# Kernel optimization log

Hardware: AMD Instinct MI355X
Metric: run time of the kernel (lower is better)

Reference implementation:

```python
import jax, jax.numpy as jnp
import numpy as np

N_NODES = 50000
N_EDGES = 800000
D = 128
L = 3


def setup_inputs() -> dict:
    key = jax.random.key(0)
    ks = jax.random.split(key, 16)
    x = jax.random.normal(ks[0], (N_NODES, D), dtype=jnp.float32)
    edge_index = jax.random.randint(ks[1], (2, N_EDGES), 0, N_NODES, dtype=jnp.int32)
    # ensure every node has at least one incoming edge (degree > 0)
    edge_index = edge_index.at[1, :N_NODES].set(jnp.arange(N_NODES, dtype=jnp.int32))
    edge_attr = jax.random.normal(ks[2], (N_EDGES, 1), dtype=jnp.float32)
    s = 1.0 / np.sqrt(D)
    lin_w = jax.random.normal(ks[3], (L, 1, D), dtype=jnp.float32)          # edge_dim=1 -> D
    lin_b = jax.random.normal(ks[4], (L, D), dtype=jnp.float32) * s
    eps = jnp.zeros((L,), dtype=jnp.float32)                                 # initial_eps = 0, trainable
    w1 = jax.random.normal(ks[5], (L, D, D), dtype=jnp.float32) * s
    b1 = jax.random.normal(ks[6], (L, D), dtype=jnp.float32) * s
    w2 = jax.random.normal(ks[7], (L, D, D), dtype=jnp.float32) * s
    b2 = jax.random.normal(ks[8], (L, D), dtype=jnp.float32) * s
    d_cat = D + L * D
    final_w = jax.random.normal(ks[9], (d_cat, D), dtype=jnp.float32) / np.sqrt(d_cat)
    final_b = jax.random.normal(ks[10], (D,), dtype=jnp.float32) * s
    return {"x": x, "edge_index": edge_index, "edge_attr": edge_attr,
            "lin_w": lin_w, "lin_b": lin_b, "eps": eps,
            "w1": w1, "b1": b1, "w2": w2, "b2": b2,
            "final_w": final_w, "final_b": final_b}


def reference(x, edge_index, edge_attr, lin_w, lin_b, eps, w1, b1, w2, b2, final_w, final_b):
    src, tgt = edge_index[0], edge_index[1]
    n = x.shape[0]
    # degree of target nodes (float), shape [N, 1]
    deg = jax.ops.segment_sum(jnp.ones(src.shape[0], x.dtype), tgt, num_segments=n)[:, None]
    xs = [x]
    h = x
    for l in range(L):
        e = edge_attr @ lin_w[l] + lin_b[l]                  # [E, D] edge-feature projection
        msg = jax.nn.relu(h[src] + e)                        # gather + fuse + relu
        agg = jax.ops.segment_sum(msg, tgt, num_segments=n)  # scatter-add
        out = agg / deg + (1.0 + eps[l]) * h                 # degree-normalize + eps-residual
        h = jax.nn.relu(out @ w1[l] + b1[l]) @ w2[l] + b2[l] # 2-layer MLP (no BN, no dropout)
        xs.append(h)
    cat = jnp.concatenate(xs, axis=-1)                       # [N, D + L*D]
    return cat @ final_w + final_b
```

## Files before the change

kernel.cpp:

```cpp
#include <hip/hip_runtime.h>

#define NN 50000
#define NE 800000
#define DIM 128
#define NLAYERS 3

typedef __attribute__((ext_vector_type(8))) short bf16x8;
typedef __attribute__((ext_vector_type(4))) float f32x4;

__device__ __forceinline__ unsigned short f2bf_hi(float f) {
    unsigned int u = __float_as_uint(f);
    u += 0x7FFF + ((u >> 16) & 1);
    return (unsigned short)(u >> 16);
}
__device__ __forceinline__ float bf2f(unsigned short u) {
    return __uint_as_float(((unsigned int)u) << 16);
}

__global__ __launch_bounds__(256) void rank_kernel(const int* __restrict__ tgt,
                                                   int* __restrict__ counts,
                                                   int* __restrict__ rank, int E) {
    int base = (blockIdx.x * 256 + threadIdx.x) * 4;
    if (base >= E) return;
    int4 t = *(const int4*)(tgt + base);
    int4 r;
    r.x = atomicAdd(&counts[t.x], 1);
    r.y = atomicAdd(&counts[t.y], 1);
    r.z = atomicAdd(&counts[t.z], 1);
    r.w = atomicAdd(&counts[t.w], 1);
    *(int4*)(rank + base) = r;
}

__global__ __launch_bounds__(256) void scan_partial_kernel(const int* __restrict__ counts,
                                                           int* __restrict__ psum, int n) {
    __shared__ int ws[4];
    int b = blockIdx.x, t = threadIdx.x;
    int idx = b * 1024 + t * 4;
    int v = 0;
    if (idx < n) {
        int4 c = *(const int4*)(counts + idx);
        v = c.x + c.y + c.z + c.w;
    }
#pragma unroll
    for (int o = 32; o > 0; o >>= 1) v += __shfl_xor(v, o);
    int lane = t & 63, wid = t >> 6;
    if (lane == 0) ws[wid] = v;
    __syncthreads();
    if (t == 0) psum[b] = ws[0] + ws[1] + ws[2] + ws[3];
}

__global__ __launch_bounds__(64) void scan_small_kernel(const int* __restrict__ psum,
                                                        int* __restrict__ pbase,
                                                        int* __restrict__ offsets,
                                                        int nb, int n) {
    int lane = threadIdx.x;
    int v = (lane < nb) ? psum[lane] : 0;
    int incl = v;
#pragma unroll
    for (int o = 1; o < 64; o <<= 1) {
        int t = __shfl_up(incl, o);
        if (lane >= o) incl += t;
    }
    if (lane < nb) pbase[lane] = incl - v;
    if (lane == 63) offsets[n] = incl;
}

__global__ __launch_bounds__(256) void scan_apply_kernel(const int* __restrict__ counts,
                                                         const int* __restrict__ pbase,
                                                         int* __restrict__ offsets, int n) {
    __shared__ int ws[4];
    int b = blockIdx.x, t = threadIdx.x;
    int lane = t & 63, wid = t >> 6;
    int idx = b * 1024 + t * 4;
    int4 c = make_int4(0, 0, 0, 0);
    if (idx < n) c = *(const int4*)(counts + idx);
    int tsum = c.x + c.y + c.z + c.w;
    int incl = tsum;
#pragma unroll
    for (int o = 1; o < 64; o <<= 1) {
        int tt = __shfl_up(incl, o);
        if (lane >= o) incl += tt;
    }
    if (lane == 63) ws[wid] = incl;
    __syncthreads();
    int wbase = pbase[b];
    for (int w = 0; w < wid; w++) wbase += ws[w];
    if (idx < n) {
        int e0 = wbase + incl - tsum;
        int4 o;
        o.x = e0;
        o.y = e0 + c.x;
        o.z = o.y + c.y;
        o.w = o.z + c.z;
        *(int4*)(offsets + idx) = o;
    }
}

__global__ __launch_bounds__(256) void scatter2_kernel(
    const int* __restrict__ src, const int* __restrict__ tgt,
    const float* __restrict__ ea, const int* __restrict__ rank,
    const int* __restrict__ offsets, int2* __restrict__ sedge, int E) {
    int base = (blockIdx.x * 256 + threadIdx.x) * 4;
    if (base >= E) return;
    int4 s = *(const int4*)(src + base);
    int4 t = *(const int4*)(tgt + base);
    int4 r = *(const int4*)(rank + base);
    float4 a = *(const float4*)(ea + base);
    sedge[offsets[t.x] + r.x] = make_int2(s.x << 8, __float_as_int(a.x));
    sedge[offsets[t.y] + r.y] = make_int2(s.y << 8, __float_as_int(a.y));
    sedge[offsets[t.z] + r.z] = make_int2(s.z << 8, __float_as_int(a.z));
    sedge[offsets[t.w] + r.w] = make_int2(s.w << 8, __float_as_int(a.w));
}

__global__ __launch_bounds__(256) void xcvt_kernel(const float* __restrict__ x,
                                                   unsigned short* __restrict__ xb, int n) {
    int i = (blockIdx.x * 256 + threadIdx.x) * 4;
    if (i >= n) return;
    float4 v = *(const float4*)(x + i);
    ushort4 o;
    o.x = f2bf_hi(v.x); o.y = f2bf_hi(v.y);
    o.z = f2bf_hi(v.z); o.w = f2bf_hi(v.w);
    *(ushort4*)(xb + i) = o;
}

__global__ __launch_bounds__(256, 8) void agg_kernel(
    const unsigned short* __restrict__ hprev, const int* __restrict__ offs,
    const int2* __restrict__ sedge,
    const float* __restrict__ lw, const float* __restrict__ lb,
    const float* __restrict__ epsp, int layer,
    unsigned short* __restrict__ aggh, unsigned short* __restrict__ aggl, int N) {
    int g = threadIdx.x >> 4;
    int r = threadIdx.x & 15;
    int node = blockIdx.x * 16 + g;
    if (node >= N) return;
    int d0 = r * 8;
    float lwv[8], lbv[8];
    *(float4*)&lwv[0] = *(const float4*)(lw + d0);
    *(float4*)&lwv[4] = *(const float4*)(lw + d0 + 4);
    *(float4*)&lbv[0] = *(const float4*)(lb + d0);
    *(float4*)&lbv[4] = *(const float4*)(lb + d0 + 4);
    const char* hb = (const char*)hprev + r * 16;

    int s0 = offs[node], s1 = offs[node + 1];
    int sm = s1 - 1;
    int cnt = s1 - s0;
    float a[8];
#pragma unroll
    for (int c = 0; c < 8; c++) a[c] = 0.f;

    int2 e0 = sedge[s0];
    int2 e1 = sedge[min(s0 + 1, sm)];
    int2 e2 = sedge[min(s0 + 2, sm)];
    int2 e3 = sedge[min(s0 + 3, sm)];
    uint4 h0 = *(const uint4*)(hb + (unsigned)e0.x);
    uint4 h1 = *(const uint4*)(hb + (unsigned)e1.x);
    uint4 h2 = *(const uint4*)(hb + (unsigned)e2.x);

    for (int it = s0; it < s1; ++it) {
        uint4 h3 = *(const uint4*)(hb + (unsigned)e3.x);
        int2 e4 = sedge[min(it + 4, sm)];
        float wgt = __int_as_float(e0.y);
        unsigned uu[4] = {h0.x, h0.y, h0.z, h0.w};
#pragma unroll
        for (int c = 0; c < 4; c++) {
            float f0 = __uint_as_float(uu[c] << 16);
            float f1 = __uint_as_float(uu[c] & 0xffff0000u);
            a[2 * c]     += fmaxf(f0 + fmaf(wgt, lwv[2 * c], lbv[2 * c]), 0.f);
            a[2 * c + 1] += fmaxf(f1 + fmaf(wgt, lwv[2 * c + 1], lbv[2 * c + 1]), 0.f);
        }
        e0 = e1; e1 = e2; e2 = e3; e3 = e4;
        h0 = h1; h1 = h2; h2 = h3;
    }

    float inv = 1.f / (float)cnt;
    float ge = 1.f + epsp[layer];
    uint4 hs = *(const uint4*)(hb + ((unsigned)node << 8));
    unsigned su[4] = {hs.x, hs.y, hs.z, hs.w};
    unsigned short hh[8], hl[8];
#pragma unroll
    for (int c = 0; c < 4; c++) {
        float f0 = __uint_as_float(su[c] << 16);
        float f1 = __uint_as_float(su[c] & 0xffff0000u);
        float v0 = a[2 * c] * inv + ge * f0;
        float v1 = a[2 * c + 1] * inv + ge * f1;
        unsigned short h0v = f2bf_hi(v0), h1v = f2bf_hi(v1);
        hh[2 * c] = h0v; hh[2 * c + 1] = h1v;
        hl[2 * c] = f2bf_hi(v0 - bf2f(h0v));
        hl[2 * c + 1] = f2bf_hi(v1 - bf2f(h1v));
    }
    unsigned short* ph = aggh + (size_t)node * DIM + d0;
    unsigned short* pl = aggl + (size_t)node * DIM + d0;
    *(ushort4*)ph       = *(const ushort4*)&hh[0];
    *(ushort4*)(ph + 4) = *(const ushort4*)&hh[4];
    *(ushort4*)pl       = *(const ushort4*)&hl[0];
    *(ushort4*)(pl + 4) = *(const ushort4*)&hl[4];
}

__device__ __forceinline__ int packidx(int k, int c) {
    return (((k >> 5) << 3) + (c >> 4)) * 512 + (((k >> 3) & 3) << 7) + ((c & 15) << 3) + (k & 7);
}

__global__ __launch_bounds__(256) void wprep_kernel(
    const float* __restrict__ w1, const float* __restrict__ w2, const float* __restrict__ fw,
    unsigned short* __restrict__ w1t_h, unsigned short* __restrict__ w1t_l,
    unsigned short* __restrict__ w2t_h, unsigned short* __restrict__ w2t_l,
    unsigned short* __restrict__ fwt_h, unsigned short* __restrict__ fwt_l) {
    int gid = blockIdx.x * 256 + threadIdx.x;
    float v; int oidx;
    unsigned short *oh, *ol;
    if (gid < 49152) {
        int l = gid >> 14, rem = gid & 16383, k = rem >> 7, c = rem & 127;
        v = w1[gid]; oidx = l * 16384 + packidx(k, c); oh = w1t_h; ol = w1t_l;
    } else if (gid < 98304) {
        int g = gid - 49152;
        int l = g >> 14, rem = g & 16383, k = rem >> 7, c = rem & 127;
        v = w2[g]; oidx = l * 16384 + packidx(k, c); oh = w2t_h; ol = w2t_l;
    } else if (gid < 163840) {
        int g = gid - 98304;
        int k = g >> 7, c = g & 127;
        v = fw[g]; oidx = packidx(k, c); oh = fwt_h; ol = fwt_l;
    } else return;
    unsigned short h = f2bf_hi(v);
    float lo = v - bf2f(h);
    oh[oidx] = h;
    ol[oidx] = f2bf_hi(lo);
}

#define HSTR 136

#define MLP1_LOAD(T, Bh_, Bl_, Ah_, Al_) do {                               \
    int k0_ = (T) * 32;                                                     \
    _Pragma("unroll")                                                       \
    for (int j_ = 0; j_ < 2; j_++) {                                        \
        size_t ro_ = (size_t)rowc[j_] * DIM + k0_ + q * 8;                  \
        Bh_[j_] = *(const bf16x8*)(ah_g + ro_);                             \
        Bl_[j_] = *(const bf16x8*)(al_g + ro_);                             \
    }                                                                       \
    _Pragma("unroll")                                                       \
    for (int i_ = 0; i_ < 4; i_++) {                                        \
        size_t co_ = ((size_t)((T) * 8 + wr * 4 + i_) << 9) + lane * 8;     \
        Ah_[i_] = *(const bf16x8*)(w1h + co_);                              \
        Al_[i_] = *(const bf16x8*)(w1l + co_);                              \
    }                                                                       \
} while (0)

#define MLP2_LOADW(T, Ah_, Al_) do {                                        \
    _Pragma("unroll")                                                       \
    for (int i_ = 0; i_ < 4; i_++) {                                        \
        size_t co_ = ((size_t)((T) * 8 + wr * 4 + i_) << 9) + lane * 8;     \
        Ah_[i_] = *(const bf16x8*)(w2h + co_);                              \
        Al_[i_] = *(const bf16x8*)(w2l + co_);                              \
    }                                                                       \
} while (0)

#define MLP2_LOADB(T, Bh_, Bl_) do {                                        \
    int k0_ = (T) * 32;                                                     \
    _Pragma("unroll")                                                       \
    for (int j_ = 0; j_ < 2; j_++) {                                        \
        int so_ = (wc * 32 + j_ * 16 + lr) * HSTR + k0_ + q * 8;            \
        Bh_[j_] = *(const bf16x8*)&s_hh[so_];                               \
        Bl_[j_] = *(const bf16x8*)&s_hl[so_];                               \
    }                                                                       \
} while (0)

#define MLP_MFMA(Bh_, Bl_, Ah_, Al_) do {                                   \
    _Pragma("unroll")                                                       \
    for (int i_ = 0; i_ < 4; i_++)                                          \
        _Pragma("unroll")                                                   \
        for (int j_ = 0; j_ < 2; j_++) {                                    \
            acc[i_][j_] = __builtin_amdgcn_mfma_f32_16x16x32_bf16(Ah_[i_], Bh_[j_], acc[i_][j_], 0, 0, 0); \
            acc[i_][j_] = __builtin_amdgcn_mfma_f32_16x16x32_bf16(Ah_[i_], Bl_[j_], acc[i_][j_], 0, 0, 0); \
            acc[i_][j_] = __builtin_amdgcn_mfma_f32_16x16x32_bf16(Al_[i_], Bh_[j_], acc[i_][j_], 0, 0, 0); \
        }                                                                   \
} while (0)

__global__ __launch_bounds__(256, 3) void mlp_fused(
    const unsigned short* __restrict__ ah_g, const unsigned short* __restrict__ al_g,
    const unsigned short* __restrict__ w1h, const unsigned short* __restrict__ w1l,
    const float* __restrict__ b1,
    const unsigned short* __restrict__ w2h, const unsigned short* __restrict__ w2l,
    const float* __restrict__ b2,
    unsigned short* __restrict__ out, int N) {
    __shared__ unsigned short s_hh[64 * HSTR], s_hl[64 * HSTR];
    int tid = threadIdx.x;
    int lane = tid & 63, w = tid >> 6;
    int q = lane >> 4, lr = lane & 15;
    int wr = w >> 1, wc = w & 1;
    int n0 = blockIdx.x * 64;
    int nb0 = n0 + wc * 32 + lr;
    int rowc[2];
    rowc[0] = min(nb0, N - 1);
    rowc[1] = min(nb0 + 16, N - 1);

    f32x4 acc[4][2];
#pragma unroll
    for (int i = 0; i < 4; i++)
#pragma unroll
        for (int j = 0; j < 2; j++) acc[i][j] = (f32x4)(0.f);

    bf16x8 pBh[2], pBl[2], pAh[4], pAl[4];
    bf16x8 qBh[2], qBl[2], qAh[4], qAl[4];

    MLP1_LOAD(0, pBh, pBl, pAh, pAl);
    MLP1_LOAD(1, qBh, qBl, qAh, qAl);
    MLP_MFMA(pBh, pBl, pAh, pAl);
    MLP1_LOAD(2, pBh, pBl, pAh, pAl);
    MLP_MFMA(qBh, qBl, qAh, qAl);
    MLP1_LOAD(3, qBh, qBl, qAh, qAl);
    MLP_MFMA(pBh, pBl, pAh, pAl);
    MLP_MFMA(qBh, qBl, qAh, qAl);

    MLP2_LOADW(0, pAh, pAl);

#pragma unroll
    for (int i = 0; i < 4; i++) {
        int hc0 = wr * 64 + i * 16 + q * 4;
        float4 bv = *(const float4*)(b1 + hc0);
        float bvr[4] = {bv.x, bv.y, bv.z, bv.w};
#pragma unroll
        for (int j = 0; j < 2; j++) {
            int nl = wc * 32 + j * 16 + lr;
            unsigned short hh[4], hl[4];
#pragma unroll
            for (int r = 0; r < 4; r++) {
                float v = fmaxf(acc[i][j][r] + bvr[r], 0.f);
                unsigned short h = f2bf_hi(v);
                hh[r] = h;
                hl[r] = f2bf_hi(v - bf2f(h));
            }
            *(ushort4*)&s_hh[nl * HSTR + hc0] = *(const ushort4*)&hh[0];
            *(ushort4*)&s_hl[nl * HSTR + hc0] = *(const ushort4*)&hl[0];
        }
    }
    __syncthreads();

#pragma unroll
    for (int i = 0; i < 4; i++)
#pragma unroll
        for (int j = 0; j < 2; j++) acc[i][j] = (f32x4)(0.f);

    MLP2_LOADB(0, pBh, pBl);
    MLP2_LOADW(1, qAh, qAl);
    MLP2_LOADB(1, qBh, qBl);
    MLP_MFMA(pBh, pBl, pAh, pAl);
    MLP2_LOADW(2, pAh, pAl);
    MLP2_LOADB(2, pBh, pBl);
    MLP_MFMA(qBh, qBl, qAh, qAl);
    MLP2_LOADW(3, qAh, qAl);
    MLP2_LOADB(3, qBh, qBl);
    MLP_MFMA(pBh, pBl, pAh, pAl);
    MLP_MFMA(qBh, qBl, qAh, qAl);

#pragma unroll
    for (int i = 0; i < 4; i++) {
        int hc0 = wr * 64 + i * 16 + q * 4;
        float4 bv = *(const float4*)(b2 + hc0);
        float bvr[4] = {bv.x, bv.y, bv.z, bv.w};
#pragma unroll
        for (int j = 0; j < 2; j++) {
            int node = nb0 + j * 16;
            if (node < N) {
                unsigned short o[4];
#pragma unroll
                for (int r = 0; r < 4; r++) o[r] = f2bf_hi(acc[i][j][r] + bvr[r]);
                *(ushort4*)&out[(size_t)node * DIM + hc0] = *(const ushort4*)&o[0];
            }
        }
    }
}

#define FIN_LOAD(T, Bv_, Ah_, Al_) do {                                     \
    const unsigned short* asrc_ = srcs[(T) >> 2];                           \
    int kk_ = ((T) & 3) * 32;                                               \
    _Pragma("unroll")                                                       \
    for (int j_ = 0; j_ < 2; j_++) {                                        \
        size_t ro_ = (size_t)rowc[j_] * DIM + kk_ + q * 8;                  \
        Bv_[j_] = *(const bf16x8*)(asrc_ + ro_);                            \
    }                                                                       \
    _Pragma("unroll")                                                       \
    for (int i_ = 0; i_ < 4; i_++) {                                        \
        size_t co_ = ((size_t)((T) * 8 + wr * 4 + i_) << 9) + lane * 8;     \
        Ah_[i_] = *(const bf16x8*)(wh + co_);                               \
        Al_[i_] = *(const bf16x8*)(wl + co_);                               \
    }                                                                       \
} while (0)

#define FIN_MFMA(Bv_, Ah_, Al_) do {                                        \
    _Pragma("unroll")                                                       \
    for (int i_ = 0; i_ < 4; i_++)                                          \
        _Pragma("unroll")                                                   \
        for (int j_ = 0; j_ < 2; j_++) {                                    \
            acc[i_][j_] = __builtin_amdgcn_mfma_f32_16x16x32_bf16(Ah_[i_], Bv_[j_], acc[i_][j_], 0, 0, 0); \
            acc[i_][j_] = __builtin_amdgcn_mfma_f32_16x16x32_bf16(Al_[i_], Bv_[j_], acc[i_][j_], 0, 0, 0); \
        }                                                                   \
} while (0)

__global__ __launch_bounds__(256, 3) void final_mfma(
    const unsigned short* __restrict__ a0, const unsigned short* __restrict__ a1,
    const unsigned short* __restrict__ a2, const unsigned short* __restrict__ a3,
    const unsigned short* __restrict__ wh, const unsigned short* __restrict__ wl,
    const float* __restrict__ bias, float* __restrict__ out, int N) {
    int tid = threadIdx.x;
    int lane = tid & 63, w = tid >> 6;
    int q = lane >> 4, lr = lane & 15;
    int wr = w >> 1, wc = w & 1;
    int n0 = blockIdx.x * 64;
    int nb0 = n0 + wc * 32 + lr;
    const unsigned short* srcs[4] = {a0, a1, a2, a3};
    int rowc[2];
    rowc[0] = min(nb0, N - 1);
    rowc[1] = min(nb0 + 16, N - 1);

    f32x4 acc[4][2];
#pragma unroll
    for (int i = 0; i < 4; i++)
#pragma unroll
        for (int j = 0; j < 2; j++) acc[i][j] = (f32x4)(0.f);

    bf16x8 pB[2], pAh[4], pAl[4];
    bf16x8 qB[2], qAh[4], qAl[4];

    FIN_LOAD(0, pB, pAh, pAl);
    FIN_LOAD(1, qB, qAh, qAl);
#pragma unroll
    for (int t = 0; t < 16; t += 2) {
        FIN_MFMA(pB, pAh, pAl);
        if (t + 2 < 16) FIN_LOAD(t + 2, pB, pAh, pAl);
        FIN_MFMA(qB, qAh, qAl);
        if (t + 3 < 16) FIN_LOAD(t + 3, qB, qAh, qAl);
    }

#pragma unroll
    for (int i = 0; i < 4; i++) {
        int hc0 = wr * 64 + i * 16 + q * 4;
        float4 bv = *(const float4*)(bias + hc0);
        float bvr[4] = {bv.x, bv.y, bv.z, bv.w};
#pragma unroll
        for (int j = 0; j < 2; j++) {
            int node = nb0 + j * 16;
            if (node < N) {
                float4 o;
                o.x = acc[i][j][0] + bvr[0];
                o.y = acc[i][j][1] + bvr[1];
                o.z = acc[i][j][2] + bvr[2];
                o.w = acc[i][j][3] + bvr[3];
                *(float4*)&out[(size_t)node * DIM + hc0] = o;
            }
        }
    }
}

extern "C" void kernel_launch(void* const* d_in, const int* in_sizes, int n_in,
                              void* d_out, int out_size, void* d_ws, size_t ws_size,
                              hipStream_t stream) {
    const float* x   = (const float*)d_in[0];
    const int* edge_index = (const int*)d_in[1];
    const float* ea  = (const float*)d_in[2];
    const float* lw  = (const float*)d_in[3];
    const float* lb  = (const float*)d_in[4];
    const float* eps = (const float*)d_in[5];
    const float* w1  = (const float*)d_in[6];
    const float* b1  = (const float*)d_in[7];
    const float* w2  = (const float*)d_in[8];
    const float* b2  = (const float*)d_in[9];
    const float* fw  = (const float*)d_in[10];
    const float* fb  = (const float*)d_in[11];
    float* out = (float*)d_out;

    const int N = NN, E = NE;
    const int* src = edge_index;
    const int* tgt = edge_index + E;
    const int NB = (N + 1023) / 1024;

    char* ws = (char*)d_ws;
    size_t off = 0;
    auto alloc = [&](size_t bytes) {
        void* p = ws + off;
        off += (bytes + 255) & ~(size_t)255;
        return p;
    };
    int*   counts  = (int*)alloc((size_t)N * 4);
    int*   offsets = (int*)alloc((size_t)(N + 1) * 4);
    int*   rank    = (int*)alloc((size_t)E * 4);
    int*   psum    = (int*)alloc((size_t)NB * 4);
    int*   pbase   = (int*)alloc((size_t)NB * 4);
    int2*  sedge   = (int2*)alloc((size_t)E * 8);
    unsigned short* w1t_h = (unsigned short*)alloc(49152 * 2);
    unsigned short* w1t_l = (unsigned short*)alloc(49152 * 2);
    unsigned short* w2t_h = (unsigned short*)alloc(49152 * 2);
    unsigned short* w2t_l = (unsigned short*)alloc(49152 * 2);
    unsigned short* fwt_h = (unsigned short*)alloc(65536 * 2);
    unsigned short* fwt_l = (unsigned short*)alloc(65536 * 2);
    unsigned short* xb    = (unsigned short*)alloc((size_t)N * DIM * 2);
    unsigned short* hbuf[3];
    for (int i = 0; i < 3; i++) hbuf[i] = (unsigned short*)alloc((size_t)N * DIM * 2);
    unsigned short* aggh = (unsigned short*)alloc((size_t)N * DIM * 2);
    unsigned short* aggl = (unsigned short*)alloc((size_t)N * DIM * 2);
    (void)ws_size; (void)in_sizes; (void)n_in; (void)out_size;

    hipMemsetAsync(counts, 0, (size_t)N * 4, stream);
    rank_kernel<<<(E / 4 + 255) / 256, 256, 0, stream>>>(tgt, counts, rank, E);
    wprep_kernel<<<640, 256, 0, stream>>>(w1, w2, fw, w1t_h, w1t_l, w2t_h, w2t_l, fwt_h, fwt_l);
    xcvt_kernel<<<(N * DIM / 4 + 255) / 256, 256, 0, stream>>>(x, xb, N * DIM);
    scan_partial_kernel<<<NB, 256, 0, stream>>>(counts, psum, N);
    scan_small_kernel<<<1, 64, 0, stream>>>(psum, pbase, offsets, NB, N);
    scan_apply_kernel<<<NB, 256, 0, stream>>>(counts, pbase, offsets, N);
    scatter2_kernel<<<(E / 4 + 255) / 256, 256, 0, stream>>>(src, tgt, ea, rank, offsets, sedge, E);

    const int GB = (N + 63) / 64;
    const int AB = (N + 15) / 16;
    for (int l = 0; l < NLAYERS; l++) {
        const unsigned short* hin = (l == 0) ? xb : hbuf[l - 1];
        agg_kernel<<<AB, 256, 0, stream>>>(hin, offsets, sedge,
            lw + l * DIM, lb + l * DIM, eps, l, aggh, aggl, N);
        mlp_fused<<<GB, 256, 0, stream>>>(
            aggh, aggl,
            w1t_h + l * 16384, w1t_l + l * 16384, b1 + l * DIM,
            w2t_h + l * 16384, w2t_l + l * 16384, b2 + l * DIM,
            hbuf[l], N);
    }
    final_mfma<<<GB, 256, 0, stream>>>(
        xb, hbuf[0], hbuf[1], hbuf[2], fwt_h, fwt_l, fb, out, N);
}
```

Baseline: 366.3 us.

## Fuse last-layer MLP with final projection and merge prep kernels

The third layer's MLP now feeds the final concat-projection directly inside one kernel. The last hidden state stays in shared memory as hi/lo bf16 and is used with split precision for the last K-slices, so it is never written to or re-read from global memory. The x conversion and weight packing kernels are also merged into one launch. This removes a kernel launch and an N×128 round trip, at the cost of a longer kernel with more register and LDS pressure, and it gives the last hidden state higher precision than the earlier layers.

```diff
diff --git a/kernel.cpp b/kernel.cpp
--- a/kernel.cpp
+++ b/kernel.cpp
@@ -112,15 +112,47 @@
     sedge[offsets[t.w] + r.w] = make_int2(s.w << 8, __float_as_int(a.w));
 }
 
-__global__ __launch_bounds__(256) void xcvt_kernel(const float* __restrict__ x,
-                                                   unsigned short* __restrict__ xb, int n) {
-    int i = (blockIdx.x * 256 + threadIdx.x) * 4;
-    if (i >= n) return;
-    float4 v = *(const float4*)(x + i);
-    ushort4 o;
-    o.x = f2bf_hi(v.x); o.y = f2bf_hi(v.y);
-    o.z = f2bf_hi(v.z); o.w = f2bf_hi(v.w);
-    *(ushort4*)(xb + i) = o;
+__device__ __forceinline__ int packidx(int k, int c) {
+    return (((k >> 5) << 3) + (c >> 4)) * 512 + (((k >> 3) & 3) << 7) + ((c & 15) << 3) + (k & 7);
+}
+
+#define XCVT_T 1600000
+
+__global__ __launch_bounds__(256) void prep_kernel(
+    const float* __restrict__ x, unsigned short* __restrict__ xb,
+    const float* __restrict__ w1, const float* __restrict__ w2, const float* __restrict__ fw,
+    unsigned short* __restrict__ w1t_h, unsigned short* __restrict__ w1t_l,
+    unsigned short* __restrict__ w2t_h, unsigned short* __restrict__ w2t_l,
+    unsigned short* __restrict__ fwt_h, unsigned short* __restrict__ fwt_l) {
+    int gid = blockIdx.x * 256 + threadIdx.x;
+    if (gid < XCVT_T) {
+        int i = gid * 4;
+        float4 v = *(const float4*)(x + i);
+        ushort4 o;
+        o.x = f2bf_hi(v.x); o.y = f2bf_hi(v.y);
+        o.z = f2bf_hi(v.z); o.w = f2bf_hi(v.w);
+        *(ushort4*)(xb + i) = o;
+        return;
+    }
+    int g0 = gid - XCVT_T;
+    float v; int oidx;
+    unsigned short *oh, *ol;
+    if (g0 < 49152) {
+        int l = g0 >> 14, rem = g0 & 16383, k = rem >> 7, c = rem & 127;
+        v = w1[g0]; oidx = l * 16384 + packidx(k, c); oh = w1t_h; ol = w1t_l;
+    } else if (g0 < 98304) {
+        int g = g0 - 49152;
+        int l = g >> 14, rem = g & 16383, k = rem >> 7, c = rem & 127;
+        v = w2[g]; oidx = l * 16384 + packidx(k, c); oh = w2t_h; ol = w2t_l;
+    } else if (g0 < 163840) {
+        int g = g0 - 98304;
+        int k = g >> 7, c = g & 127;
+        v = fw[g]; oidx = packidx(k, c); oh = fwt_h; ol = fwt_l;
+    } else return;
+    unsigned short h = f2bf_hi(v);
+    float lo = v - bf2f(h);
+    oh[oidx] = h;
+    ol[oidx] = f2bf_hi(lo);
 }
 
 __global__ __launch_bounds__(256, 8) void agg_kernel(
@@ -196,36 +228,6 @@
     *(ushort4*)(pl + 4) = *(const ushort4*)&hl[4];
 }
 
-__device__ __forceinline__ int packidx(int k, int c) {
-    return (((k >> 5) << 3) + (c >> 4)) * 512 + (((k >> 3) & 3) << 7) + ((c & 15) << 3) + (k & 7);
-}
-
-__global__ __launch_bounds__(256) void wprep_kernel(
-    const float* __restrict__ w1, const float* __restrict__ w2, const float* __restrict__ fw,
-    unsigned short* __restrict__ w1t_h, unsigned short* __restrict__ w1t_l,
-    unsigned short* __restrict__ w2t_h, unsigned short* __restrict__ w2t_l,
-    unsigned short* __restrict__ fwt_h, unsigned short* __restrict__ fwt_l) {
-    int gid = blockIdx.x * 256 + threadIdx.x;
-    float v; int oidx;
-    unsigned short *oh, *ol;
-    if (gid < 49152) {
-        int l = gid >> 14, rem = gid & 16383, k = rem >> 7, c = rem & 127;
-        v = w1[gid]; oidx = l * 16384 + packidx(k, c); oh = w1t_h; ol = w1t_l;
-    } else if (gid < 98304) {
-        int g = gid - 49152;
-        int l = g >> 14, rem = g & 16383, k = rem >> 7, c = rem & 127;
-        v = w2[g]; oidx = l * 16384 + packidx(k, c); oh = w2t_h; ol = w2t_l;
-    } else if (gid < 163840) {
-        int g = gid - 98304;
-        int k = g >> 7, c = g & 127;
-        v = fw[g]; oidx = packidx(k, c); oh = fwt_h; ol = fwt_l;
-    } else return;
-    unsigned short h = f2bf_hi(v);
-    float lo = v - bf2f(h);
-    oh[oidx] = h;
-    ol[oidx] = f2bf_hi(lo);
-}
-
 #define HSTR 136
 
 #define MLP1_LOAD(T, Bh_, Bl_, Ah_, Al_) do {                               \
@@ -273,6 +275,60 @@
             acc[i_][j_] = __builtin_amdgcn_mfma_f32_16x16x32_bf16(Al_[i_], Bh_[j_], acc[i_][j_], 0, 0, 0); \
         }                                                                   \
 } while (0)
+
+#define MLP_PHASES_12()                                                     \
+    f32x4 acc[4][2];                                                        \
+    _Pragma("unroll")                                                       \
+    for (int i = 0; i < 4; i++)                                             \
+        _Pragma("unroll")                                                   \
+        for (int j = 0; j < 2; j++) acc[i][j] = (f32x4)(0.f);               \
+    bf16x8 pBh[2], pBl[2], pAh[4], pAl[4];                                  \
+    bf16x8 qBh[2], qBl[2], qAh[4], qAl[4];                                  \
+    MLP1_LOAD(0, pBh, pBl, pAh, pAl);                                       \
+    MLP1_LOAD(1, qBh, qBl, qAh, qAl);                                       \
+    MLP_MFMA(pBh, pBl, pAh, pAl);                                           \
+    MLP1_LOAD(2, pBh, pBl, pAh, pAl);                                       \
+    MLP_MFMA(qBh, qBl, qAh, qAl);                                           \
+    MLP1_LOAD(3, qBh, qBl, qAh, qAl);                                       \
+    MLP_MFMA(pBh, pBl, pAh, pAl);                                           \
+    MLP_MFMA(qBh, qBl, qAh, qAl);                                           \
+    MLP2_LOADW(0, pAh, pAl);                                                \
+    _Pragma("unroll")                                                       \
+    for (int i = 0; i < 4; i++) {                                           \
+        int hc0 = wr * 64 + i * 16 + q * 4;                                 \
+        float4 bv = *(const float4*)(b1 + hc0);                             \
+        float bvr[4] = {bv.x, bv.y, bv.z, bv.w};                            \
+        _Pragma("unroll")                                                   \
+        for (int j = 0; j < 2; j++) {                                       \
+            int nl = wc * 32 + j * 16 + lr;                                 \
+            unsigned short hh[4], hl[4];                                    \
+            _Pragma("unroll")                                               \
+            for (int r = 0; r < 4; r++) {                                   \
+                float v = fmaxf(acc[i][j][r] + bvr[r], 0.f);                \
+                unsigned short h = f2bf_hi(v);                              \
+                hh[r] = h;                                                  \
+                hl[r] = f2bf_hi(v - bf2f(h));                               \
+            }                                                               \
+            *(ushort4*)&s_hh[nl * HSTR + hc0] = *(const ushort4*)&hh[0];    \
+            *(ushort4*)&s_hl[nl * HSTR + hc0] = *(const ushort4*)&hl[0];    \
+        }                                                                   \
+    }                                                                       \
+    __syncthreads();                                                        \
+    _Pragma("unroll")                                                       \
+    for (int i = 0; i < 4; i++)                                             \
+        _Pragma("unroll")                                                   \
+        for (int j = 0; j < 2; j++) acc[i][j] = (f32x4)(0.f);               \
+    MLP2_LOADB(0, pBh, pBl);                                                \
+    MLP2_LOADW(1, qAh, qAl);                                                \
+    MLP2_LOADB(1, qBh, qBl);                                                \
+    MLP_MFMA(pBh, pBl, pAh, pAl);                                           \
+    MLP2_LOADW(2, pAh, pAl);                                                \
+    MLP2_LOADB(2, pBh, pBl);                                                \
+    MLP_MFMA(qBh, qBl, qAh, qAl);                                           \
+    MLP2_LOADW(3, qAh, qAl);                                                \
+    MLP2_LOADB(3, qBh, qBl);                                                \
+    MLP_MFMA(pBh, pBl, pAh, pAl);                                           \
+    MLP_MFMA(qBh, qBl, qAh, qAl);
 
 __global__ __launch_bounds__(256, 3) void mlp_fused(
     const unsigned short* __restrict__ ah_g, const unsigned short* __restrict__ al_g,
@@ -292,30 +348,106 @@
     rowc[0] = min(nb0, N - 1);
     rowc[1] = min(nb0 + 16, N - 1);
 
-    f32x4 acc[4][2];
-#pragma unroll
-    for (int i = 0; i < 4; i++)
-#pragma unroll
-        for (int j = 0; j < 2; j++) acc[i][j] = (f32x4)(0.f);
-
-    bf16x8 pBh[2], pBl[2], pAh[4], pAl[4];
-    bf16x8 qBh[2], qBl[2], qAh[4], qAl[4];
-
-    MLP1_LOAD(0, pBh, pBl, pAh, pAl);
-    MLP1_LOAD(1, qBh, qBl, qAh, qAl);
-    MLP_MFMA(pBh, pBl, pAh, pAl);
-    MLP1_LOAD(2, pBh, pBl, pAh, pAl);
-    MLP_MFMA(qBh, qBl, qAh, qAl);
-    MLP1_LOAD(3, qBh, qBl, qAh, qAl);
-    MLP_MFMA(pBh, pBl, pAh, pAl);
-    MLP_MFMA(qBh, qBl, qAh, qAl);
-
-    MLP2_LOADW(0, pAh, pAl);
+    MLP_PHASES_12();
 
 #pragma unroll
     for (int i = 0; i < 4; i++) {
         int hc0 = wr * 64 + i * 16 + q * 4;
-        float4 bv = *(const float4*)(b1 + hc0);
+        float4 bv = *(const float4*)(b2 + hc0);
+        float bvr[4] = {bv.x, bv.y, bv.z, bv.w};
+#pragma unroll
+        for (int j = 0; j < 2; j++) {
+            int node = nb0 + j * 16;
+            if (node < N) {
+                unsigned short o[4];
+#pragma unroll
+                for (int r = 0; r < 4; r++) o[r] = f2bf_hi(acc[i][j][r] + bvr[r]);
+                *(ushort4*)&out[(size_t)node * DIM + hc0] = *(const ushort4*)&o[0];
+            }
+        }
+    }
+}
+
+#define FIN3_LOADG(T, Bv_, Ah_, Al_) do {                                   \
+    const unsigned short* asrc_ = srcs3[(T) >> 2];                          \
+    int kk_ = ((T) & 3) * 32;                                               \
+    _Pragma("unroll")                                                       \
+    for (int j_ = 0; j_ < 2; j_++) {                                        \
+        size_t ro_ = (size_t)rowc[j_] * DIM + kk_ + q * 8;                  \
+        Bv_[j_] = *(const bf16x8*)(asrc_ + ro_);                            \
+    }                                                                       \
+    _Pragma("unroll")                                                       \
+    for (int i_ = 0; i_ < 4; i_++) {                                        \
+        size_t co_ = ((size_t)((T) * 8 + wr * 4 + i_) << 9) + lane * 8;     \
+        Ah_[i_] = *(const bf16x8*)(fwh + co_);                              \
+        Al_[i_] = *(const bf16x8*)(fwl + co_);                              \
+    }                                                                       \
+} while (0)
+
+#define FIN_MFMA(Bv_, Ah_, Al_) do {                                        \
+    _Pragma("unroll")                                                       \
+    for (int i_ = 0; i_ < 4; i_++)                                          \
+        _Pragma("unroll")                                                   \
+        for (int j_ = 0; j_ < 2; j_++) {                                    \
+            acc[i_][j_] = __builtin_amdgcn_mfma_f32_16x16x32_bf16(Ah_[i_], Bv_[j_], acc[i_][j_], 0, 0, 0); \
+            acc[i_][j_] = __builtin_amdgcn_mfma_f32_16x16x32_bf16(Al_[i_], Bv_[j_], acc[i_][j_], 0, 0, 0); \
+        }                                                                   \
+} while (0)
+
+#define FIN3_STEPL(T) do {                                                  \
+    int kk_ = ((T) - 12) * 32;                                              \
+    bf16x8 Bh_[2], Bl_[2], Ah_[4], Al_[4];                                  \
+    _Pragma("unroll")                                                       \
+    for (int j_ = 0; j_ < 2; j_++) {                                        \
+        int so_ = (wc * 32 + j_ * 16 + lr) * HSTR + kk_ + q * 8;            \
+        Bh_[j_] = *(const bf16x8*)&s_hh[so_];                               \
+        Bl_[j_] = *(const bf16x8*)&s_hl[so_];                               \
+    }                                                                       \
+    _Pragma("unroll")                                                       \
+    for (int i_ = 0; i_ < 4; i_++) {                                        \
+        size_t co_ = ((size_t)((T) * 8 + wr * 4 + i_) << 9) + lane * 8;     \
+        Ah_[i_] = *(const bf16x8*)(fwh + co_);                              \
+        Al_[i_] = *(const bf16x8*)(fwl + co_);                              \
+    }                                                                       \
+    _Pragma("unroll")                                                       \
+    for (int i_ = 0; i_ < 4; i_++)                                          \
+        _Pragma("unroll")                                                   \
+        for (int j_ = 0; j_ < 2; j_++) {                                    \
+            acc[i_][j_] = __builtin_amdgcn_mfma_f32_16x16x32_bf16(Ah_[i_], Bh_[j_], acc[i_][j_], 0, 0, 0); \
+            acc[i_][j_] = __builtin_amdgcn_mfma_f32_16x16x32_bf16(Ah_[i_], Bl_[j_], acc[i_][j_], 0, 0, 0); \
+            acc[i_][j_] = __builtin_amdgcn_mfma_f32_16x16x32_bf16(Al_[i_], Bh_[j_], acc[i_][j_], 0, 0, 0); \
+        }                                                                   \
+} while (0)
+
+__global__ __launch_bounds__(256, 3) void mlp_final_fused(
+    const unsigned short* __restrict__ ah_g, const unsigned short* __restrict__ al_g,
+    const unsigned short* __restrict__ w1h, const unsigned short* __restrict__ w1l,
+    const float* __restrict__ b1,
+    const unsigned short* __restrict__ w2h, const unsigned short* __restrict__ w2l,
+    const float* __restrict__ b2,
+    const unsigned short* __restrict__ xsrc, const unsigned short* __restrict__ h0p,
+    const unsigned short* __restrict__ h1p,
+    const unsigned short* __restrict__ fwh, const unsigned short* __restrict__ fwl,
+    const float* __restrict__ fbias, float* __restrict__ out, int N) {
+    __shared__ unsigned short s_hh[64 * HSTR], s_hl[64 * HSTR];
+    int tid = threadIdx.x;
+    int lane = tid & 63, w = tid >> 6;
+    int q = lane >> 4, lr = lane & 15;
+    int wr = w >> 1, wc = w & 1;
+    int n0 = blockIdx.x * 64;
+    int nb0 = n0 + wc * 32 + lr;
+    int rowc[2];
+    rowc[0] = min(nb0, N - 1);
+    rowc[1] = min(nb0 + 16, N - 1);
+
+    MLP_PHASES_12();
+
+    __syncthreads();
+
+#pragma unroll
+    for (int i = 0; i < 4; i++) {
+        int hc0 = wr * 64 + i * 16 + q * 4;
+        float4 bv = *(const float4*)(b2 + hc0);
         float bvr[4] = {bv.x, bv.y, bv.z, bv.w};
 #pragma unroll
         for (int j = 0; j < 2; j++) {
@@ -323,7 +455,7 @@
             unsigned short hh[4], hl[4];
 #pragma unroll
             for (int r = 0; r < 4; r++) {
-                float v = fmaxf(acc[i][j][r] + bvr[r], 0.f);
+                float v = acc[i][j][r] + bvr[r];
                 unsigned short h = f2bf_hi(v);
                 hh[r] = h;
                 hl[r] = f2bf_hi(v - bf2f(h));
@@ -332,108 +464,35 @@
             *(ushort4*)&s_hl[nl * HSTR + hc0] = *(const ushort4*)&hl[0];
         }
     }
+
+#pragma unroll
+    for (int i = 0; i < 4; i++)
+#pragma unroll
+        for (int j = 0; j < 2; j++) acc[i][j] = (f32x4)(0.f);
+
+    const unsigned short* srcs3[3] = {xsrc, h0p, h1p};
+    bf16x8 pB[2], pWh[4], pWl[4];
+    bf16x8 qB[2], qWh[4], qWl[4];
+    FIN3_LOADG(0, pB, pWh, pWl);
+    FIN3_LOADG(1, qB, qWh, qWl);
     __syncthreads();
 
 #pragma unroll
-    for (int i = 0; i < 4; i++)
-#pragma unroll
-        for (int j = 0; j < 2; j++) acc[i][j] = (f32x4)(0.f);
-
-    MLP2_LOADB(0, pBh, pBl);
-    MLP2_LOADW(1, qAh, qAl);
-    MLP2_LOADB(1, qBh, qBl);
-    MLP_MFMA(pBh, pBl, pAh, pAl);
-    MLP2_LOADW(2, pAh, pAl);
-    MLP2_LOADB(2, pBh, pBl);
-    MLP_MFMA(qBh, qBl, qAh, qAl);
-    MLP2_LOADW(3, qAh, qAl);
-    MLP2_LOADB(3, qBh, qBl);
-    MLP_MFMA(pBh, pBl, pAh, pAl);
-    MLP_MFMA(qBh, qBl, qAh, qAl);
+    for (int t = 0; t < 12; t += 2) {
+        FIN_MFMA(pB, pWh, pWl);
+        if (t + 2 < 12) FIN3_LOADG(t + 2, pB, pWh, pWl);
+        FIN_MFMA(qB, qWh, qWl);
+        if (t + 3 < 12) FIN3_LOADG(t + 3, qB, qWh, qWl);
+    }
+    FIN3_STEPL(12);
+    FIN3_STEPL(13);
+    FIN3_STEPL(14);
+    FIN3_STEPL(15);
 
 #pragma unroll
     for (int i = 0; i < 4; i++) {
         int hc0 = wr * 64 + i * 16 + q * 4;
-        float4 bv = *(const float4*)(b2 + hc0);
-        float bvr[4] = {bv.x, bv.y, bv.z, bv.w};
-#pragma unroll
-        for (int j = 0; j < 2; j++) {
-            int node = nb0 + j * 16;
-            if (node < N) {
-                unsigned short o[4];
-#pragma unroll
-                for (int r = 0; r < 4; r++) o[r] = f2bf_hi(acc[i][j][r] + bvr[r]);
-                *(ushort4*)&out[(size_t)node * DIM + hc0] = *(const ushort4*)&o[0];
-            }
-        }
-    }
-}
-
-#define FIN_LOAD(T, Bv_, Ah_, Al_) do {                                     \
-    const unsigned short* asrc_ = srcs[(T) >> 2];                           \
-    int kk_ = ((T) & 3) * 32;                                               \
-    _Pragma("unroll")                                                       \
-    for (int j_ = 0; j_ < 2; j_++) {                                        \
-        size_t ro_ = (size_t)rowc[j_] * DIM + kk_ + q * 8;                  \
-        Bv_[j_] = *(const bf16x8*)(asrc_ + ro_);                            \
-    }                                                                       \
-    _Pragma("unroll")                                                       \
-    for (int i_ = 0; i_ < 4; i_++) {                                        \
-        size_t co_ = ((size_t)((T) * 8 + wr * 4 + i_) << 9) + lane * 8;     \
-        Ah_[i_] = *(const bf16x8*)(wh + co_);                               \
-        Al_[i_] = *(const bf16x8*)(wl + co_);                               \
-    }                                                                       \
-} while (0)
-
-#define FIN_MFMA(Bv_, Ah_, Al_) do {                                        \
-    _Pragma("unroll")                                                       \
-    for (int i_ = 0; i_ < 4; i_++)                                          \
-        _Pragma("unroll")                                                   \
-        for (int j_ = 0; j_ < 2; j_++) {                                    \
-            acc[i_][j_] = __builtin_amdgcn_mfma_f32_16x16x32_bf16(Ah_[i_], Bv_[j_], acc[i_][j_], 0, 0, 0); \
-            acc[i_][j_] = __builtin_amdgcn_mfma_f32_16x16x32_bf16(Al_[i_], Bv_[j_], acc[i_][j_], 0, 0, 0); \
-        }                                                                   \
-} while (0)
-
-__global__ __launch_bounds__(256, 3) void final_mfma(
-    const unsigned short* __restrict__ a0, const unsigned short* __restrict__ a1,
-    const unsigned short* __restrict__ a2, const unsigned short* __restrict__ a3,
-    const unsigned short* __restrict__ wh, const unsigned short* __restrict__ wl,
-    const float* __restrict__ bias, float* __restrict__ out, int N) {
-    int tid = threadIdx.x;
-    int lane = tid & 63, w = tid >> 6;
-    int q = lane >> 4, lr = lane & 15;
-    int wr = w >> 1, wc = w & 1;
-    int n0 = blockIdx.x * 64;
-    int nb0 = n0 + wc * 32 + lr;
-    const unsigned short* srcs[4] = {a0, a1, a2, a3};
-    int rowc[2];
-    rowc[0] = min(nb0, N - 1);
-    rowc[1] = min(nb0 + 16, N - 1);
-
-    f32x4 acc[4][2];
-#pragma unroll
-    for (int i = 0; i < 4; i++)
-#pragma unroll
-        for (int j = 0; j < 2; j++) acc[i][j] = (f32x4)(0.f);
-
-    bf16x8 pB[2], pAh[4], pAl[4];
-    bf16x8 qB[2], qAh[4], qAl[4];
-
-    FIN_LOAD(0, pB, pAh, pAl);
-    FIN_LOAD(1, qB, qAh, qAl);
-#pragma unroll
-    for (int t = 0; t < 16; t += 2) {
-        FIN_MFMA(pB, pAh, pAl);
-        if (t + 2 < 16) FIN_LOAD(t + 2, pB, pAh, pAl);
-        FIN_MFMA(qB, qAh, qAl);
-        if (t + 3 < 16) FIN_LOAD(t + 3, qB, qAh, qAl);
-    }
-
-#pragma unroll
-    for (int i = 0; i < 4; i++) {
-        int hc0 = wr * 64 + i * 16 + q * 4;
-        float4 bv = *(const float4*)(bias + hc0);
+        float4 bv = *(const float4*)(fbias + hc0);
         float bvr[4] = {bv.x, bv.y, bv.z, bv.w};
 #pragma unroll
         for (int j = 0; j < 2; j++) {
@@ -492,16 +551,16 @@
     unsigned short* fwt_h = (unsigned short*)alloc(65536 * 2);
     unsigned short* fwt_l = (unsigned short*)alloc(65536 * 2);
     unsigned short* xb    = (unsigned short*)alloc((size_t)N * DIM * 2);
-    unsigned short* hbuf[3];
-    for (int i = 0; i < 3; i++) hbuf[i] = (unsigned short*)alloc((size_t)N * DIM * 2);
+    unsigned short* hbuf[2];
+    for (int i = 0; i < 2; i++) hbuf[i] = (unsigned short*)alloc((size_t)N * DIM * 2);
     unsigned short* aggh = (unsigned short*)alloc((size_t)N * DIM * 2);
     unsigned short* aggl = (unsigned short*)alloc((size_t)N * DIM * 2);
     (void)ws_size; (void)in_sizes; (void)n_in; (void)out_size;
 
     hipMemsetAsync(counts, 0, (size_t)N * 4, stream);
     rank_kernel<<<(E / 4 + 255) / 256, 256, 0, stream>>>(tgt, counts, rank, E);
-    wprep_kernel<<<640, 256, 0, stream>>>(w1, w2, fw, w1t_h, w1t_l, w2t_h, w2t_l, fwt_h, fwt_l);
-    xcvt_kernel<<<(N * DIM / 4 + 255) / 256, 256, 0, stream>>>(x, xb, N * DIM);
+    prep_kernel<<<(XCVT_T + 163840 + 255) / 256, 256, 0, stream>>>(
+        x, xb, w1, w2, fw, w1t_h, w1t_l, w2t_h, w2t_l, fwt_h, fwt_l);
     scan_partial_kernel<<<NB, 256, 0, stream>>>(counts, psum, N);
     scan_small_kernel<<<1, 64, 0, stream>>>(psum, pbase, offsets, NB, N);
     scan_apply_kernel<<<NB, 256, 0, stream>>>(counts, pbase, offsets, N);
@@ -509,7 +568,7 @@
 
     const int GB = (N + 63) / 64;
     const int AB = (N + 15) / 16;
-    for (int l = 0; l < NLAYERS; l++) {
+    for (int l = 0; l < 2; l++) {
         const unsigned short* hin = (l == 0) ? xb : hbuf[l - 1];
         agg_kernel<<<AB, 256, 0, stream>>>(hin, offsets, sedge,
             lw + l * DIM, lb + l * DIM, eps, l, aggh, aggl, N);
@@ -519,6 +578,11 @@
             w2t_h + l * 16384, w2t_l + l * 16384, b2 + l * DIM,
             hbuf[l], N);
     }
-    final_mfma<<<GB, 256, 0, stream>>>(
-        xb, hbuf[0], hbuf[1], hbuf[2], fwt_h, fwt_l, fb, out, N);
-}
+    agg_kernel<<<AB, 256, 0, stream>>>(hbuf[1], offsets, sedge,
+        lw + 2 * DIM, lb + 2 * DIM, eps, 2, aggh, aggl, N);
+    mlp_final_fused<<<GB, 256, 0, stream>>>(
+        aggh, aggl,
+        w1t_h + 2 * 16384, w1t_l + 2 * 16384, b1 + 2 * DIM,
+        w2t_h + 2 * 16384, w2t_l + 2 * 16384, b2 + 2 * DIM,
+        xb, hbuf[0], hbuf[1], fwt_h, fwt_l, fb, out, N);
+}
```

After: 354.2 us. -3.3%, faster.
